# Performance work log

Hardware: AMD Instinct MI355X
Metric: run time of the kernel (lower is better)

The kernel has to match this reference:

```python
import jax, jax.numpy as jnp
import numpy as np

B, C, N = 2, 128, 784  # batch, channels, spatial tokens (28x28)
TEMPERATURE = 11.313708498984761  # sqrt(C)


def setup_inputs() -> dict:
    key = jax.random.key(0)
    kq, kk, kv = jax.random.split(key, 3)
    q = jax.random.normal(kq, (B, C, N), dtype=jnp.float32)
    k = jax.random.normal(kk, (B, C, N), dtype=jnp.float32)
    v = jax.random.normal(kv, (B, C, N), dtype=jnp.float32)
    return {"q": q, "k": k, "v": v}


def reference(q, k, v):
    # dist_func == 'l1' branch of ScaledDotProductAttention (eval mode, dropout=0)
    qs = q / TEMPERATURE                                   # [B, C, Nq]
    # torch: q.unsqueeze(2).repeat -> [B,C,Nk,Nq]; k.unsqueeze(3).repeat -> [B,C,Nk,Nq]
    # broadcast instead of repeat; mean over channel dim 1
    diff = jnp.abs(qs[:, :, None, :] - k[:, :, :, None])   # [B, C, Nk, Nq]
    attn = jnp.mean(diff, axis=1)                          # [B, Nk, Nq]
    attn = jax.nn.softmax(attn, axis=-1)                   # softmax over Nq (last dim)
    # torch.bmm(v, attn.permute(0,2,1)): out[b,c,k] = sum_q v[b,c,q] * attn[b,k,q]
    out = jnp.einsum("bcq,bkq->bck", v, attn)              # [B, C, Nk]
    return (out, attn)
```

## Files before the change

kernel.cpp:

```cpp
#include <hip/hip_runtime.h>
#include <math.h>

constexpr int kB = 2;
constexpr int kC = 128;
constexpr int kN = 784;
constexpr float kInvT = 1.0f / 11.313708498984761f;
constexpr float kInvC = 1.0f / 128.0f;

constexpr size_t kOutElems  = (size_t)kB * kC * kN;
constexpr size_t kAttnElems = (size_t)kB * kN * kN;

__device__ inline float wave_max(float v) {
#pragma unroll
    for (int o = 32; o > 0; o >>= 1) v = fmaxf(v, __shfl_xor(v, o, 64));
    return v;
}
__device__ inline float wave_sum(float v) {
#pragma unroll
    for (int o = 32; o > 0; o >>= 1) v += __shfl_xor(v, o, 64);
    return v;
}

constexpr int TK = 64;
constexpr int TQ = 64;
constexpr int NKT = (kN + TK - 1) / TK;
constexpr int NQT = (kN + TQ - 1) / TQ;
constexpr int CSP = 2;
constexpr int CH = kC / CSP;
constexpr int DSTR = 68;

template <bool USE_WS>
__global__ __launch_bounds__(256) void dist_kernel(const float* __restrict__ qg,
                                                   const float* __restrict__ kg,
                                                   float* __restrict__ D0,
                                                   float* __restrict__ D1) {
    int bid = blockIdx.x;
    const int qt = bid % NQT; bid /= NQT;
    const int kt = bid % NKT; bid /= NKT;
    const int ch = bid & 1;   bid >>= 1;
    const int b  = bid;
    const int k0 = kt * TK;
    const int q0 = qt * TQ;
    const int t  = threadIdx.x;

    __shared__ float ks[CH][DSTR];
    __shared__ float qs[CH][DSTR];

    const float* kb = kg + ((size_t)b * kC + ch * CH) * kN;
    const float* qb = qg + ((size_t)b * kC + ch * CH) * kN;

#pragma unroll
    for (int i = t; i < CH * 16; i += 256) {
        const int c  = i >> 4;
        const int x4 = (i & 15) << 2;
        *reinterpret_cast<float4*>(&ks[c][x4]) =
            *reinterpret_cast<const float4*>(kb + (size_t)c * kN + min(k0 + x4, kN - 4));
        float4 qv = *reinterpret_cast<const float4*>(qb + (size_t)c * kN + min(q0 + x4, kN - 4));
        qv.x *= kInvT; qv.y *= kInvT; qv.z *= kInvT; qv.w *= kInvT;
        *reinterpret_cast<float4*>(&qs[c][x4]) = qv;
    }
    __syncthreads();

    const int qx = (t & 15) << 2;
    const int kx = (t >> 4) << 2;

    float acc[4][4];
#pragma unroll
    for (int i = 0; i < 4; ++i)
#pragma unroll
        for (int j = 0; j < 4; ++j) acc[i][j] = 0.0f;

#pragma unroll 4
    for (int c = 0; c < CH; ++c) {
        const float4 kv = *reinterpret_cast<const float4*>(&ks[c][kx]);
        const float4 qv = *reinterpret_cast<const float4*>(&qs[c][qx]);
        const float kf[4] = {kv.x, kv.y, kv.z, kv.w};
        const float qf[4] = {qv.x, qv.y, qv.z, qv.w};
#pragma unroll
        for (int i = 0; i < 4; ++i)
#pragma unroll
            for (int j = 0; j < 4; ++j)
                acc[i][j] += fabsf(qf[j] - kf[i]);
    }

    const int qcol = q0 + qx;
    if (qcol < kN) {
        float* dst = (USE_WS && ch) ? D1 : D0;
#pragma unroll
        for (int i = 0; i < 4; ++i) {
            const int krow = k0 + kx + i;
            if (krow < kN) {
                const size_t off = ((size_t)b * kN + krow) * kN + qcol;
                if (USE_WS) {
                    *reinterpret_cast<float4*>(dst + off) =
                        make_float4(acc[i][0], acc[i][1], acc[i][2], acc[i][3]);
                } else {
                    atomicAdd(&D0[off + 0], acc[i][0]);
                    atomicAdd(&D0[off + 1], acc[i][1]);
                    atomicAdd(&D0[off + 2], acc[i][2]);
                    atomicAdd(&D0[off + 3], acc[i][3]);
                }
            }
        }
    }
}

template <bool SUM2>
__global__ __launch_bounds__(256) void softmax_kernel(float* __restrict__ A,
                                                      const float* __restrict__ W) {
    const size_t row = (size_t)blockIdx.x * kN;
    float4* A4 = reinterpret_cast<float4*>(A + row);
    const float4* W4 = reinterpret_cast<const float4*>(W + row);
    const int t = threadIdx.x;
    const int lane = t & 63, wid = t >> 6;
    const bool act = t < (kN / 4);
    __shared__ float xred[4];

    float4 x = make_float4(-1e30f, -1e30f, -1e30f, -1e30f);
    if (act) {
        x = A4[t];
        if (SUM2) {
            const float4 w = W4[t];
            x.x += w.x; x.y += w.y; x.z += w.z; x.w += w.w;
        }
    }

    float m = fmaxf(fmaxf(x.x, x.y), fmaxf(x.z, x.w));
    m = wave_max(m);
    if (lane == 0) xred[wid] = m;
    __syncthreads();
    m = fmaxf(fmaxf(xred[0], xred[1]), fmaxf(xred[2], xred[3]));
    __syncthreads();

    float4 p;
    p.x = __expf((x.x - m) * kInvC);
    p.y = __expf((x.y - m) * kInvC);
    p.z = __expf((x.z - m) * kInvC);
    p.w = __expf((x.w - m) * kInvC);
    float lsum = p.x + p.y + p.z + p.w;
    lsum = wave_sum(lsum);
    if (lane == 0) xred[wid] = lsum;
    __syncthreads();
    const float inv = 1.0f / (xred[0] + xred[1] + xred[2] + xred[3]);
    if (act) {
        p.x *= inv; p.y *= inv; p.z *= inv; p.w *= inv;
        A4[t] = p;
    }
}

typedef _Float16 half8v __attribute__((ext_vector_type(8)));
typedef float f32x4 __attribute__((ext_vector_type(4)));

constexpr int GN = 64;
constexpr int GK = 128;
constexpr int QSP3 = (kN + GK - 1) / GK;
constexpr int NKT3 = (kN + GN - 1) / GN;

__device__ inline half8v to_h8(const float4 a, const float4 b) {
    half8v h;
    h[0] = (_Float16)a.x; h[1] = (_Float16)a.y; h[2] = (_Float16)a.z; h[3] = (_Float16)a.w;
    h[4] = (_Float16)b.x; h[5] = (_Float16)b.y; h[6] = (_Float16)b.z; h[7] = (_Float16)b.w;
    return h;
}

template <bool ATOMIC>
__global__ __launch_bounds__(256) void bmm_mfma(const float* __restrict__ vg,
                                                const float* __restrict__ attn,
                                                float* __restrict__ P) {
    int bid = blockIdx.x;
    const int qs = bid % QSP3; bid /= QSP3;
    const int kt = bid % NKT3; bid /= NKT3;
    const int ct = bid & 1;    bid >>= 1;
    const int b  = bid;
    const int k0 = kt * GN;
    const int c0 = ct * 64;
    const int q0 = qs * GK;
    const int t  = threadIdx.x;
    const int lane = t & 63;
    const int w = t >> 6;

    const int lrow = lane & 15;
    const int kgrp = (lane >> 4) * 8;

    const float* vp = vg + (((size_t)b * kC + c0 + 16 * w + lrow) * kN + q0 + kgrp);
    const float* ap[4];
#pragma unroll
    for (int n = 0; n < 4; ++n) {
        const int krow = min(k0 + 16 * n + lrow, kN - 1);
        ap[n] = attn + (((size_t)b * kN + krow) * kN + q0 + kgrp);
    }

    f32x4 acc[4] = {};

    if (q0 + GK <= kN) {
#pragma unroll
        for (int ks = 0; ks < GK / 32; ++ks) {
            const int qb = ks * 32;
            const half8v av = to_h8(*reinterpret_cast<const float4*>(vp + qb),
                                    *reinterpret_cast<const float4*>(vp + qb + 4));
#pragma unroll
            for (int n = 0; n < 4; ++n) {
                const half8v bv = to_h8(*reinterpret_cast<const float4*>(ap[n] + qb),
                                        *reinterpret_cast<const float4*>(ap[n] + qb + 4));
                acc[n] = __builtin_amdgcn_mfma_f32_16x16x32_f16(av, bv, acc[n], 0, 0, 0);
            }
        }
    } else {
        const float4 z = make_float4(0.f, 0.f, 0.f, 0.f);
        const bool ok = (q0 + kgrp) < kN;
        const half8v av = to_h8(ok ? *reinterpret_cast<const float4*>(vp) : z,
                                ok ? *reinterpret_cast<const float4*>(vp + 4) : z);
#pragma unroll
        for (int n = 0; n < 4; ++n) {
            const half8v bv = to_h8(ok ? *reinterpret_cast<const float4*>(ap[n]) : z,
                                    ok ? *reinterpret_cast<const float4*>(ap[n] + 4) : z);
            acc[n] = __builtin_amdgcn_mfma_f32_16x16x32_f16(av, bv, acc[n], 0, 0, 0);
        }
    }

    const int crow = c0 + 16 * w + (lane >> 4) * 4;
    const int kc = k0 + lrow;
#pragma unroll
    for (int n = 0; n < 4; ++n) {
        const int kcol = kc + 16 * n;
        if (kcol < kN) {
            if (ATOMIC) {
#pragma unroll
                for (int r = 0; r < 4; ++r)
                    atomicAdd(&P[((size_t)b * kC + crow + r) * kN + kcol], acc[n][r]);
            } else {
                float* op = P + (((size_t)qs * kB + b) * kC + crow) * kN + kcol;
#pragma unroll
                for (int r = 0; r < 4; ++r) op[(size_t)r * kN] = acc[n][r];
            }
        }
    }
}

__global__ __launch_bounds__(256) void reduce_kernel(const float* __restrict__ P,
                                                     float* __restrict__ out) {
    const int idx = blockIdx.x * 256 + threadIdx.x;
    const float4* p = reinterpret_cast<const float4*>(P) + idx;
    float4 s = p[0];
#pragma unroll
    for (int qs = 1; qs < QSP3; ++qs) {
        const float4 v = p[(size_t)qs * (kOutElems / 4)];
        s.x += v.x; s.y += v.y; s.z += v.z; s.w += v.w;
    }
    reinterpret_cast<float4*>(out)[idx] = s;
}

extern "C" void kernel_launch(void* const* d_in, const int* in_sizes, int n_in,
                              void* d_out, int out_size, void* d_ws, size_t ws_size,
                              hipStream_t stream) {
    const float* q = (const float*)d_in[0];
    const float* k = (const float*)d_in[1];
    const float* v = (const float*)d_in[2];

    float* out  = (float*)d_out;
    float* attn = out + kOutElems;
    float* D1   = (float*)d_ws;
    float* P    = D1 + kAttnElems;

    const size_t need = (kAttnElems + (size_t)QSP3 * kOutElems) * sizeof(float);

    if (ws_size >= need) {
        dist_kernel<true><<<kB * CSP * NKT * NQT, 256, 0, stream>>>(q, k, attn, D1);
        softmax_kernel<true><<<kB * kN, 256, 0, stream>>>(attn, D1);
        bmm_mfma<false><<<kB * 2 * NKT3 * QSP3, 256, 0, stream>>>(v, attn, P);
        reduce_kernel<<<(int)(kOutElems / 4 / 256), 256, 0, stream>>>(P, out);
    } else {
        hipMemsetAsync(attn, 0, kAttnElems * sizeof(float), stream);
        hipMemsetAsync(out, 0, kOutElems * sizeof(float), stream);
        dist_kernel<false><<<kB * CSP * NKT * NQT, 256, 0, stream>>>(q, k, attn, nullptr);
        softmax_kernel<false><<<kB * kN, 256, 0, stream>>>(attn, attn);
        bmm_mfma<true><<<kB * 2 * NKT3 * QSP3, 256, 0, stream>>>(v, attn, out);
    }
}
```

Measured before the change: 94.84 us.

## Compute L1 distances with packed fp16 math and drop channel split

Rewrites the distance kernel to convert q and k to fp16 in shared memory and accumulate |q-k| with packed half2 subtract, abs-by-mask and add. Partial fp16 sums over 32-channel segments are flushed to fp32. The channel split with its second workspace buffer and the summing softmax pass are removed, so the full channel reduction happens in one block. This cuts ALU work and memory traffic, at the cost of fp16 rounding in the distances that then feed the softmax.

```diff
diff --git a/kernel.cpp b/kernel.cpp
--- a/kernel.cpp
+++ b/kernel.cpp
@@ -10,6 +10,13 @@
 constexpr size_t kOutElems  = (size_t)kB * kC * kN;
 constexpr size_t kAttnElems = (size_t)kB * kN * kN;
 
+typedef _Float16 h2 __attribute__((ext_vector_type(2)));
+typedef _Float16 half8v __attribute__((ext_vector_type(8)));
+typedef float f32x4 __attribute__((ext_vector_type(4)));
+
+__device__ inline h2 u2h(unsigned u) { union { unsigned u; h2 h; } x; x.u = u; return x.h; }
+__device__ inline unsigned h2u(h2 h) { union { unsigned u; h2 h; } x; x.h = h; return x.u; }
+
 __device__ inline float wave_max(float v) {
 #pragma unroll
     for (int o = 32; o > 0; o >>= 1) v = fmaxf(v, __shfl_xor(v, o, 64));
@@ -21,109 +28,105 @@
     return v;
 }
 
-constexpr int TK = 64;
-constexpr int TQ = 64;
-constexpr int NKT = (kN + TK - 1) / TK;
-constexpr int NQT = (kN + TQ - 1) / TQ;
-constexpr int CSP = 2;
-constexpr int CH = kC / CSP;
-constexpr int DSTR = 68;
-
-template <bool USE_WS>
+constexpr int TKD = 32;
+constexpr int TQD = 64;
+constexpr int NKTD = (kN + TKD - 1) / TKD;
+constexpr int NQTD = (kN + TQD - 1) / TQD;
+constexpr int KSTR = 32;
+
 __global__ __launch_bounds__(256) void dist_kernel(const float* __restrict__ qg,
                                                    const float* __restrict__ kg,
-                                                   float* __restrict__ D0,
-                                                   float* __restrict__ D1) {
+                                                   float* __restrict__ D) {
     int bid = blockIdx.x;
-    const int qt = bid % NQT; bid /= NQT;
-    const int kt = bid % NKT; bid /= NKT;
-    const int ch = bid & 1;   bid >>= 1;
+    const int qt = bid % NQTD; bid /= NQTD;
+    const int kt = bid % NKTD; bid /= NKTD;
     const int b  = bid;
-    const int k0 = kt * TK;
-    const int q0 = qt * TQ;
+    const int k0 = kt * TKD;
+    const int q0 = qt * TQD;
     const int t  = threadIdx.x;
 
-    __shared__ float ks[CH][DSTR];
-    __shared__ float qs[CH][DSTR];
-
-    const float* kb = kg + ((size_t)b * kC + ch * CH) * kN;
-    const float* qb = qg + ((size_t)b * kC + ch * CH) * kN;
-
-#pragma unroll
-    for (int i = t; i < CH * 16; i += 256) {
-        const int c  = i >> 4;
-        const int x4 = (i & 15) << 2;
-        *reinterpret_cast<float4*>(&ks[c][x4]) =
-            *reinterpret_cast<const float4*>(kb + (size_t)c * kN + min(k0 + x4, kN - 4));
-        float4 qv = *reinterpret_cast<const float4*>(qb + (size_t)c * kN + min(q0 + x4, kN - 4));
+    __shared__ unsigned ks2[kC][KSTR];
+    __shared__ unsigned qs2[kC][KSTR];
+
+    const float* kb = kg + (size_t)b * kC * kN;
+    const float* qb = qg + (size_t)b * kC * kN;
+
+#pragma unroll
+    for (int i = t; i < kC * 8; i += 256) {
+        const int c = i >> 3, g = i & 7;
+        const float4 kv =
+            *reinterpret_cast<const float4*>(kb + (size_t)c * kN + min(k0 + 4 * g, kN - 4));
+        uint4 d;
+        h2 p;
+        p[0] = p[1] = (_Float16)kv.x; d.x = h2u(p);
+        p[0] = p[1] = (_Float16)kv.y; d.y = h2u(p);
+        p[0] = p[1] = (_Float16)kv.z; d.z = h2u(p);
+        p[0] = p[1] = (_Float16)kv.w; d.w = h2u(p);
+        *reinterpret_cast<uint4*>(&ks2[c][4 * g]) = d;
+    }
+#pragma unroll
+    for (int i = t; i < kC * 16; i += 256) {
+        const int c = i >> 4, g = i & 15;
+        float4 qv =
+            *reinterpret_cast<const float4*>(qb + (size_t)c * kN + min(q0 + 4 * g, kN - 4));
         qv.x *= kInvT; qv.y *= kInvT; qv.z *= kInvT; qv.w *= kInvT;
-        *reinterpret_cast<float4*>(&qs[c][x4]) = qv;
-    }
-    __syncthreads();
-
-    const int qx = (t & 15) << 2;
-    const int kx = (t >> 4) << 2;
-
-    float acc[4][4];
-#pragma unroll
-    for (int i = 0; i < 4; ++i)
-#pragma unroll
-        for (int j = 0; j < 4; ++j) acc[i][j] = 0.0f;
-
-#pragma unroll 4
-    for (int c = 0; c < CH; ++c) {
-        const float4 kv = *reinterpret_cast<const float4*>(&ks[c][kx]);
-        const float4 qv = *reinterpret_cast<const float4*>(&qs[c][qx]);
-        const float kf[4] = {kv.x, kv.y, kv.z, kv.w};
-        const float qf[4] = {qv.x, qv.y, qv.z, qv.w};
-#pragma unroll
-        for (int i = 0; i < 4; ++i)
-#pragma unroll
-            for (int j = 0; j < 4; ++j)
-                acc[i][j] += fabsf(qf[j] - kf[i]);
-    }
-
-    const int qcol = q0 + qx;
+        uint2 d;
+        h2 p;
+        p[0] = (_Float16)qv.x; p[1] = (_Float16)qv.y; d.x = h2u(p);
+        p[0] = (_Float16)qv.z; p[1] = (_Float16)qv.w; d.y = h2u(p);
+        *reinterpret_cast<uint2*>(&qs2[c][2 * g]) = d;
+    }
+    __syncthreads();
+
+    const int qgp = t & 31;
+    const int kx  = t >> 5;
+
+    float accM[4][2];
+#pragma unroll
+    for (int j = 0; j < 4; ++j) accM[j][0] = accM[j][1] = 0.0f;
+
+#pragma unroll
+    for (int seg = 0; seg < 4; ++seg) {
+        h2 a0 = u2h(0), a1 = u2h(0), a2 = u2h(0), a3 = u2h(0);
+#pragma unroll
+        for (int cc = 0; cc < 32; ++cc) {
+            const int c = seg * 32 + cc;
+            const uint4 kd = *reinterpret_cast<const uint4*>(&ks2[c][4 * kx]);
+            const h2 qp = u2h(qs2[c][qgp]);
+            a0 += u2h(h2u(qp - u2h(kd.x)) & 0x7FFF7FFFu);
+            a1 += u2h(h2u(qp - u2h(kd.y)) & 0x7FFF7FFFu);
+            a2 += u2h(h2u(qp - u2h(kd.z)) & 0x7FFF7FFFu);
+            a3 += u2h(h2u(qp - u2h(kd.w)) & 0x7FFF7FFFu);
+        }
+        accM[0][0] += (float)a0[0]; accM[0][1] += (float)a0[1];
+        accM[1][0] += (float)a1[0]; accM[1][1] += (float)a1[1];
+        accM[2][0] += (float)a2[0]; accM[2][1] += (float)a2[1];
+        accM[3][0] += (float)a3[0]; accM[3][1] += (float)a3[1];
+    }
+
+    const int qcol = q0 + 2 * qgp;
     if (qcol < kN) {
-        float* dst = (USE_WS && ch) ? D1 : D0;
-#pragma unroll
-        for (int i = 0; i < 4; ++i) {
-            const int krow = k0 + kx + i;
+#pragma unroll
+        for (int j = 0; j < 4; ++j) {
+            const int krow = k0 + 4 * kx + j;
             if (krow < kN) {
-                const size_t off = ((size_t)b * kN + krow) * kN + qcol;
-                if (USE_WS) {
-                    *reinterpret_cast<float4*>(dst + off) =
-                        make_float4(acc[i][0], acc[i][1], acc[i][2], acc[i][3]);
-                } else {
-                    atomicAdd(&D0[off + 0], acc[i][0]);
-                    atomicAdd(&D0[off + 1], acc[i][1]);
-                    atomicAdd(&D0[off + 2], acc[i][2]);
-                    atomicAdd(&D0[off + 3], acc[i][3]);
-                }
+                *reinterpret_cast<float2*>(&D[((size_t)b * kN + krow) * kN + qcol]) =
+                    make_float2(accM[j][0], accM[j][1]);
             }
         }
     }
 }
 
-template <bool SUM2>
-__global__ __launch_bounds__(256) void softmax_kernel(float* __restrict__ A,
-                                                      const float* __restrict__ W) {
+__global__ __launch_bounds__(256) void softmax_kernel(float* __restrict__ A) {
     const size_t row = (size_t)blockIdx.x * kN;
     float4* A4 = reinterpret_cast<float4*>(A + row);
-    const float4* W4 = reinterpret_cast<const float4*>(W + row);
     const int t = threadIdx.x;
     const int lane = t & 63, wid = t >> 6;
     const bool act = t < (kN / 4);
     __shared__ float xred[4];
 
     float4 x = make_float4(-1e30f, -1e30f, -1e30f, -1e30f);
-    if (act) {
-        x = A4[t];
-        if (SUM2) {
-            const float4 w = W4[t];
-            x.x += w.x; x.y += w.y; x.z += w.z; x.w += w.w;
-        }
-    }
+    if (act) x = A4[t];
 
     float m = fmaxf(fmaxf(x.x, x.y), fmaxf(x.z, x.w));
     m = wave_max(m);
@@ -147,9 +150,6 @@
         A4[t] = p;
     }
 }
-
-typedef _Float16 half8v __attribute__((ext_vector_type(8)));
-typedef float f32x4 __attribute__((ext_vector_type(4)));
 
 constexpr int GN = 64;
 constexpr int GK = 128;
@@ -259,21 +259,19 @@
 
     float* out  = (float*)d_out;
     float* attn = out + kOutElems;
-    float* D1   = (float*)d_ws;
-    float* P    = D1 + kAttnElems;
-
-    const size_t need = (kAttnElems + (size_t)QSP3 * kOutElems) * sizeof(float);
+    float* P    = (float*)d_ws;
+
+    const size_t need = (size_t)QSP3 * kOutElems * sizeof(float);
 
     if (ws_size >= need) {
-        dist_kernel<true><<<kB * CSP * NKT * NQT, 256, 0, stream>>>(q, k, attn, D1);
-        softmax_kernel<true><<<kB * kN, 256, 0, stream>>>(attn, D1);
+        dist_kernel<<<kB * NKTD * NQTD, 256, 0, stream>>>(q, k, attn);
+        softmax_kernel<<<kB * kN, 256, 0, stream>>>(attn);
         bmm_mfma<false><<<kB * 2 * NKT3 * QSP3, 256, 0, stream>>>(v, attn, P);
         reduce_kernel<<<(int)(kOutElems / 4 / 256), 256, 0, stream>>>(P, out);
     } else {
-        hipMemsetAsync(attn, 0, kAttnElems * sizeof(float), stream);
         hipMemsetAsync(out, 0, kOutElems * sizeof(float), stream);
-        dist_kernel<false><<<kB * CSP * NKT * NQT, 256, 0, stream>>>(q, k, attn, nullptr);
-        softmax_kernel<false><<<kB * kN, 256, 0, stream>>>(attn, attn);
+        dist_kernel<<<kB * NKTD * NQTD, 256, 0, stream>>>(q, k, attn);
+        softmax_kernel<<<kB * kN, 256, 0, stream>>>(attn);
         bmm_mfma<true><<<kB * 2 * NKT3 * QSP3, 256, 0, stream>>>(v, attn, out);
     }
 }
```

After: 117.3 us. 1.24x slower.
